# Optimization experiments

Measured on AMD Instinct MI355X. Metric: run time of the kernel, lower is better.

## Reference

```python
import jax, jax.numpy as jnp
import numpy as np

B, T, L, H, W = 8, 30000, 6, 128, 128
D_IN, C_DIM, HID, Z_DIM = 3, 32, 256, 128
MAX_DIM = 0.55


def setup_inputs() -> dict:
    key = jax.random.key(0)
    ks = jax.random.split(key, 12)
    p = jax.random.uniform(ks[0], (B, T, D_IN), dtype=jnp.float32)
    z = jax.random.normal(ks[1], (B, Z_DIM), dtype=jnp.float32)
    c = jax.random.normal(ks[2], (B, L, H, W, C_DIM), dtype=jnp.float32)
    # camera-like matrices: small rotation rows so projected coords stay in [-1, 1]
    C_mat = (jax.random.uniform(ks[3], (B, L, 4, 3), dtype=jnp.float32) - 0.5) * 0.3
    C_mat = C_mat.at[:, :, 3, :].set(1.0)  # row used as projection denominator
    fc_p_w = jax.random.normal(ks[4], (HID, D_IN), dtype=jnp.float32) * 0.1
    fc_p_b = jnp.zeros((HID,), jnp.float32)
    blk0_w0 = jax.random.normal(ks[5], (C_DIM, HID), dtype=jnp.float32) * 0.05
    blk0_b0 = jnp.zeros((C_DIM,), jnp.float32)
    blk0_w1 = jax.random.normal(ks[6], (C_DIM, C_DIM), dtype=jnp.float32) * 0.1
    blk0_b1 = jnp.zeros((C_DIM,), jnp.float32)
    blk0_ws = jax.random.normal(ks[7], (C_DIM, HID), dtype=jnp.float32) * 0.05
    blk_w0 = jax.random.normal(ks[8], (4, C_DIM, C_DIM), dtype=jnp.float32) * 0.1
    blk_b0 = jnp.zeros((4, C_DIM), jnp.float32)
    blk_w1 = jax.random.normal(ks[9], (4, C_DIM, C_DIM), dtype=jnp.float32) * 0.1
    blk_b1 = jnp.zeros((4, C_DIM), jnp.float32)
    fc_out_w = jax.random.normal(ks[10], (1, C_DIM), dtype=jnp.float32) * 0.1
    fc_out_b = jnp.zeros((1,), jnp.float32)
    return dict(p=p, z=z, c=c, C_mat=C_mat, fc_p_w=fc_p_w, fc_p_b=fc_p_b,
                blk0_w0=blk0_w0, blk0_b0=blk0_b0, blk0_w1=blk0_w1, blk0_b1=blk0_b1,
                blk0_ws=blk0_ws, blk_w0=blk_w0, blk_b0=blk_b0, blk_w1=blk_w1,
                blk_b1=blk_b1, fc_out_w=fc_out_w, fc_out_b=fc_out_b)


def _bilinear(p, c, C_mat):
    # p: [B,T,3], c: [B,L,H,W,D], C_mat: [B,L,4,3]
    Bb, Ll, Hh, Ww, Dd = c.shape
    interval = 2.0 / (Hh - 1)
    pp = p / MAX_DIM
    # proj[b,l,t,i] = sum_j C_mat[b,l,i,j] * pp[b,t,j]
    proj = jnp.einsum('blij,btj->blti', C_mat[:, :, :3, :], pp)
    denom = C_mat[:, :, 3, 0] + 0.05                      # [B,L]
    proj = proj / denom[:, :, None, None]
    xy = (proj[..., :2] + 1.0) / interval                 # [B,L,T,2]
    x, y = xy[..., 0], xy[..., 1]
    x0f, x1f = jnp.floor(x), jnp.ceil(x)
    y0f, y1f = jnp.floor(y), jnp.ceil(y)
    dx = (x1f - x)[..., None]                             # [B,L,T,1]
    dy = (y1f - y)[..., None]
    x0 = jnp.clip(x0f.astype(jnp.int32), 0, Hh - 1)
    x1 = jnp.clip(x1f.astype(jnp.int32), 0, Hh - 1)
    y0 = jnp.clip(y0f.astype(jnp.int32), 0, Ww - 1)
    y1 = jnp.clip(y1f.astype(jnp.int32), 0, Ww - 1)
    bi = jnp.arange(Bb)[:, None, None]
    li = jnp.arange(Ll)[None, :, None]
    f11 = c[bi, li, x0, y0]                               # [B,L,T,D]
    f12 = c[bi, li, x1, y0]
    f21 = c[bi, li, x0, y1]
    f22 = c[bi, li, x1, y1]
    interp = (f11 * dx * dy + f12 * (1 - dx) * dy
              + f21 * dx * (1 - dy) + f22 * (1 - dx) * (1 - dy))
    return interp.sum(axis=1)                             # sum over views -> [B,T,D]


def reference(p, z, c, C_mat, fc_p_w, fc_p_b, blk0_w0, blk0_b0, blk0_w1, blk0_b1,
              blk0_ws, blk_w0, blk_b0, blk_w1, blk_b1, fc_out_w, fc_out_b):
    feat = _bilinear(p, c, C_mat)                         # [B,T,32]
    net = p @ fc_p_w.T + fc_p_b                           # 1x1 conv == linear, [B,T,256]
    # block0 (256 -> 32, with linear shortcut)
    h = jax.nn.relu(net) @ blk0_w0.T + blk0_b0
    dx_ = jax.nn.relu(h) @ blk0_w1.T + blk0_b1
    net = net @ blk0_ws.T + dx_
    net = net + feat
    # blocks 1..4 (32 -> 32, identity shortcut)
    for i in range(4):
        h = jax.nn.relu(net) @ blk_w0[i].T + blk_b0[i]
        net = net + (jax.nn.relu(h) @ blk_w1[i].T + blk_b1[i])
        net = net + feat
    out = jax.nn.relu(net) @ fc_out_w.T + fc_out_b        # [B,T,1]
    return out[..., 0]                                    # [B,T]
```

## Files before the change

### kernel.cpp

```cpp
#include <hip/hip_runtime.h>

#define NB 8
#define NT 30000
#define NL 6
#define NC 32
#define NHID 256

typedef _Float16 f16;
typedef f16 half8 __attribute__((ext_vector_type(8)));
typedef f16 half4v __attribute__((ext_vector_type(4)));
typedef f16 half2v __attribute__((ext_vector_type(2)));
typedef float floatx4 __attribute__((ext_vector_type(4)));

__device__ __forceinline__ int permrow(int m) {
    return 8 * ((m & 15) >> 2) + 4 * (m >> 4) + (m & 3);
}

__device__ __forceinline__ half2v cvt2(float a, float b) {
    return __builtin_bit_cast(half2v, __builtin_amdgcn_cvt_pkrtz(a, b));
}

__device__ __forceinline__ half8 relupack2(floatx4 a, floatx4 b) {
    half2v p0 = cvt2(fmaxf(a[0], 0.f), fmaxf(a[1], 0.f));
    half2v p1 = cvt2(fmaxf(a[2], 0.f), fmaxf(a[3], 0.f));
    half2v p2 = cvt2(fmaxf(b[0], 0.f), fmaxf(b[1], 0.f));
    half2v p3 = cvt2(fmaxf(b[2], 0.f), fmaxf(b[3], 0.f));
    half4v q0 = __builtin_shufflevector(p0, p1, 0, 1, 2, 3);
    half4v q1 = __builtin_shufflevector(p2, p3, 0, 1, 2, 3);
    return __builtin_shufflevector(q0, q1, 0, 1, 2, 3, 4, 5, 6, 7);
}

__device__ __forceinline__ half8 zext4(half4v lo) {
    const half4v zh = {};
    return __builtin_shufflevector(lo, zh, 0, 1, 2, 3, 4, 5, 6, 7);
}

__global__ void fold_kernel(const float* __restrict__ ws, const float* __restrict__ fpw,
                            const float* __restrict__ fpb, floatx4* __restrict__ out) {
    __shared__ floatx4 s_part[8][32];
    int tid = threadIdx.x;
    int i = tid & 31, kc = tid >> 5;
    const float* wrow = ws + i * 256 + kc * 32;
    const float* pw = fpw + kc * 96;
    const float* pb = fpb + kc * 32;
    floatx4 acc = {};
    #pragma unroll 8
    for (int k = 0; k < 32; k++) {
        float w = wrow[k];
        acc[0] = fmaf(w, pw[k * 3 + 0], acc[0]);
        acc[1] = fmaf(w, pw[k * 3 + 1], acc[1]);
        acc[2] = fmaf(w, pw[k * 3 + 2], acc[2]);
        acc[3] = fmaf(w, pb[k], acc[3]);
    }
    s_part[kc][i] = acc;
    __syncthreads();
    if (kc == 0) {
        floatx4 s = s_part[0][i];
        #pragma unroll
        for (int j = 1; j < 8; j++) s += s_part[j][i];
        out[i] = s;
    }
}

__launch_bounds__(256, 2)
__global__ void decoder_kernel(
    const float* __restrict__ p, const float* __restrict__ c, const float* __restrict__ Cm,
    const float* __restrict__ fpw, const float* __restrict__ fpb,
    const float* __restrict__ b0w0, const float* __restrict__ b0b0,
    const float* __restrict__ b0w1, const float* __restrict__ b0b1,
    const float* __restrict__ bw0, const float* __restrict__ bb0,
    const float* __restrict__ bw1, const float* __restrict__ bb1,
    const float* __restrict__ fow, const float* __restrict__ fob,
    const floatx4* __restrict__ fold, float* __restrict__ out)
{
    __shared__ __align__(16) f16 s_w0A[32 * 256];
    __shared__ __align__(16) f16 s_wA[9 * 32 * 32];
    __shared__ __align__(16) f16 s_hB[256 * 4];
    __shared__ __align__(16) f16 s_foldA[32 * 4];
    __shared__ __align__(16) float s_b0b0[32], s_fow[32];
    __shared__ __align__(16) float s_bb0f[128], s_bb1f[128];
    __shared__ float s_cam[NL][8];
    __shared__ float s_fob;

    const int tid = threadIdx.x;
    const int b = blockIdx.y;

    {
        int m = tid >> 3, seg = tid & 7;
        const float* src = b0w0 + permrow(m) * 256 + seg * 32;
        f16* dst = s_w0A + m * 256;
        int sw = m & 7;
        #pragma unroll
        for (int ci = 0; ci < 4; ci++) {
            int cidx = seg * 4 + ci;
            floatx4 f0 = *(const floatx4*)(src + ci * 8);
            floatx4 f1 = *(const floatx4*)(src + ci * 8 + 4);
            half2v h0 = cvt2(f0[0], f0[1]), h1 = cvt2(f0[2], f0[3]);
            half2v h2 = cvt2(f1[0], f1[1]), h3 = cvt2(f1[2], f1[3]);
            half4v q0 = __builtin_shufflevector(h0, h1, 0, 1, 2, 3);
            half4v q1 = __builtin_shufflevector(h2, h3, 0, 1, 2, 3);
            half8 h = __builtin_shufflevector(q0, q1, 0, 1, 2, 3, 4, 5, 6, 7);
            *(half8*)(dst + ((cidx ^ sw) << 3)) = h;
        }
    }
    for (int r = tid; r < 288; r += 256) {
        int mi = r >> 5, m = r & 31;
        int pm = permrow(m);
        const float* src;
        if (mi == 0) src = b0w1 + pm * 32;
        else {
            int mat = mi - 1, bi = mat >> 1;
            src = ((mat & 1) ? bw1 : bw0) + (bi * 32 + pm) * 32;
        }
        f16* dst = s_wA + mi * 1024 + m * 32;
        int sw = (m >> 1) & 3;
        #pragma unroll
        for (int ci = 0; ci < 4; ci++) {
            floatx4 f0 = *(const floatx4*)(src + ci * 8);
            floatx4 f1 = *(const floatx4*)(src + ci * 8 + 4);
            half2v h0 = cvt2(f0[0], f0[1]), h1 = cvt2(f0[2], f0[3]);
            half2v h2 = cvt2(f1[0], f1[1]), h3 = cvt2(f1[2], f1[3]);
            half4v q0 = __builtin_shufflevector(h0, h1, 0, 1, 2, 3);
            half4v q1 = __builtin_shufflevector(h2, h3, 0, 1, 2, 3);
            half8 h = __builtin_shufflevector(q0, q1, 0, 1, 2, 3, 4, 5, 6, 7);
            *(half8*)(dst + ((ci ^ sw) << 3)) = h;
        }
    }
    {
        int cch = tid >> 5, m = tid & 31;
        int h = cch * 32 + permrow(m);
        half2v a = cvt2(fpw[h * 3 + 0], fpw[h * 3 + 1]);
        half2v bq = cvt2(fpw[h * 3 + 2], fpb[h]);
        *(half4v*)(s_hB + tid * 4) = __builtin_shufflevector(a, bq, 0, 1, 2, 3);
    }
    if (tid < 32) {
        int pm = permrow(tid);
        floatx4 f = fold[pm];
        half2v a = cvt2(f[0], f[1]);
        half2v bq = cvt2(f[2], f[3] + b0b1[pm]);
        *(half4v*)(s_foldA + tid * 4) = __builtin_shufflevector(a, bq, 0, 1, 2, 3);
        s_b0b0[tid] = b0b0[tid];
        s_fow[tid]  = fow[tid];
    }
    if (tid >= 64 && tid < 192) {
        int j = tid - 64;
        s_bb0f[j] = bb0[j];
        s_bb1f[j] = bb1[j];
    }
    if (tid == 0) s_fob = fob[0];
    if (tid >= 192 && tid < 192 + NL) {
        int l = tid - 192;
        const float* cm = Cm + ((size_t)b * NL + l) * 12;
        float denom = cm[9] + 0.05f;
        float s = 63.5f / (0.55f * denom);
        s_cam[l][0] = cm[0] * s; s_cam[l][1] = cm[1] * s; s_cam[l][2] = cm[2] * s;
        s_cam[l][3] = cm[3] * s; s_cam[l][4] = cm[4] * s; s_cam[l][5] = cm[5] * s;
    }
    __syncthreads();

    const int lane = tid & 63;
    const int wv = tid >> 6;
    const int q = lane >> 4;
    const int i16 = lane & 15;
    const int sw0 = i16 & 7;

    const f16* w0r0 = s_w0A + i16 * 256;
    const f16* w0r1 = s_w0A + (16 + i16) * 256;
    const int qsw = (q ^ ((i16 >> 1) & 3)) << 3;
    const int soff0 = i16 * 32 + qsw;
    const int soff1 = (16 + i16) * 32 + qsw;
    const f16* hB0 = s_hB + i16 * 4;
    const f16* hB1 = s_hB + (16 + i16) * 4;
    const float* cq = c + (((size_t)b * NL) << 19) + q * 8;

    const half8 fA0 = zext4(*(const half4v*)(s_foldA + i16 * 4));
    const half8 fA1 = zext4(*(const half4v*)(s_foldA + (16 + i16) * 4));
    const floatx4 fw0 = *(const floatx4*)&s_fow[q * 8];
    const floatx4 fw1 = *(const floatx4*)&s_fow[q * 8 + 4];
    const floatx4 b00a = *(const floatx4*)&s_b0b0[q * 8];
    const floatx4 b00b = *(const floatx4*)&s_b0b0[q * 8 + 4];

    #pragma unroll 1
    for (int g = 0; g < 2; g++) {
        const int t = blockIdx.x * 128 + (g * 4 + wv) * 16 + i16;
        const int tc = min(t, NT - 1);
        const float* pp = p + ((size_t)b * NT + tc) * 3;
        float px = pp[0], py = pp[1], pz = pp[2];

        floatx4 fe0 = {}, fe1 = {};
        #pragma unroll 1
        for (int l = 0; l < NL; l++) {
            float x = s_cam[l][0] * px + s_cam[l][1] * py + s_cam[l][2] * pz + 63.5f;
            float y = s_cam[l][3] * px + s_cam[l][4] * py + s_cam[l][5] * pz + 63.5f;
            float x0f = floorf(x), x1f = ceilf(x);
            float y0f = floorf(y), y1f = ceilf(y);
            float dxw = x1f - x, dyw = y1f - y;
            int x0 = min(max((int)x0f, 0), 127);
            int x1 = min(max((int)x1f, 0), 127);
            int y0 = min(max((int)y0f, 0), 127);
            int y1 = min(max((int)y1f, 0), 127);
            const float* base = cq + ((size_t)l << 19);
            const floatx4* f11 = (const floatx4*)(base + (size_t)((x0 << 7) + y0) * 32);
            const floatx4* f12 = (const floatx4*)(base + (size_t)((x1 << 7) + y0) * 32);
            const floatx4* f21 = (const floatx4*)(base + (size_t)((x0 << 7) + y1) * 32);
            const floatx4* f22 = (const floatx4*)(base + (size_t)((x1 << 7) + y1) * 32);
            float w11 = dxw * dyw;
            float w12 = (1.f - dxw) * dyw;
            float w21 = dxw * (1.f - dyw);
            float w22 = (1.f - dxw) * (1.f - dyw);
            floatx4 a0 = f11[0], a1 = f11[1];
            floatx4 b0v = f12[0], b1v = f12[1];
            floatx4 c0v = f21[0], c1v = f21[1];
            floatx4 d0v = f22[0], d1v = f22[1];
            fe0 += a0 * w11 + b0v * w12 + c0v * w21 + d0v * w22;
            fe1 += a1 * w11 + b1v * w12 + c1v * w21 + d1v * w22;
        }

        half8 bp;
        {
            half2v xy = cvt2(px, py), z1 = cvt2(pz, 1.0f);
            half4v lo = __builtin_shufflevector(xy, z1, 0, 1, 2, 3);
            half8 full = zext4(lo);
            const half8 zh8 = {};
            bp = (q == 0) ? full : zh8;
        }

        floatx4 acc0 = b00a, acc1 = b00b;
        #pragma unroll 2
        for (int cch = 0; cch < 8; cch++) {
            half8 ha = zext4(*(const half4v*)(hB0 + cch * 128));
            half8 hb = zext4(*(const half4v*)(hB1 + cch * 128));
            floatx4 hz = {};
            floatx4 h0 = __builtin_amdgcn_mfma_f32_16x16x32_f16(ha, bp, hz, 0, 0, 0);
            floatx4 h1 = __builtin_amdgcn_mfma_f32_16x16x32_f16(hb, bp, hz, 0, 0, 0);
            half8 bf = relupack2(h0, h1);
            half8 a0 = *(const half8*)(w0r0 + ((((cch << 2) | q) ^ sw0) << 3));
            half8 a1 = *(const half8*)(w0r1 + ((((cch << 2) | q) ^ sw0) << 3));
            acc0 = __builtin_amdgcn_mfma_f32_16x16x32_f16(a0, bf, acc0, 0, 0, 0);
            acc1 = __builtin_amdgcn_mfma_f32_16x16x32_f16(a1, bf, acc1, 0, 0, 0);
        }

        floatx4 st0 = __builtin_amdgcn_mfma_f32_16x16x32_f16(fA0, bp, fe0, 0, 0, 0);
        floatx4 st1 = __builtin_amdgcn_mfma_f32_16x16x32_f16(fA1, bp, fe1, 0, 0, 0);
        {
            half8 bf = relupack2(acc0, acc1);
            half8 a0 = *(const half8*)(s_wA + soff0);
            half8 a1 = *(const half8*)(s_wA + soff1);
            st0 = __builtin_amdgcn_mfma_f32_16x16x32_f16(a0, bf, st0, 0, 0, 0);
            st1 = __builtin_amdgcn_mfma_f32_16x16x32_f16(a1, bf, st1, 0, 0, 0);
        }

        #pragma unroll
        for (int bk = 0; bk < 4; bk++) {
            const f16* w_a = s_wA + (1 + 2 * bk) * 1024;
            const f16* w_b = s_wA + (2 + 2 * bk) * 1024;
            floatx4 h0 = *(const floatx4*)&s_bb0f[bk * 32 + q * 8];
            floatx4 h1 = *(const floatx4*)&s_bb0f[bk * 32 + q * 8 + 4];
            {
                half8 bf = relupack2(st0, st1);
                half8 a0 = *(const half8*)(w_a + soff0);
                half8 a1 = *(const half8*)(w_a + soff1);
                h0 = __builtin_amdgcn_mfma_f32_16x16x32_f16(a0, bf, h0, 0, 0, 0);
                h1 = __builtin_amdgcn_mfma_f32_16x16x32_f16(a1, bf, h1, 0, 0, 0);
            }
            floatx4 d0 = *(const floatx4*)&s_bb1f[bk * 32 + q * 8];
            floatx4 d1 = *(const floatx4*)&s_bb1f[bk * 32 + q * 8 + 4];
            {
                half8 bf = relupack2(h0, h1);
                half8 a0 = *(const half8*)(w_b + soff0);
                half8 a1 = *(const half8*)(w_b + soff1);
                d0 = __builtin_amdgcn_mfma_f32_16x16x32_f16(a0, bf, d0, 0, 0, 0);
                d1 = __builtin_amdgcn_mfma_f32_16x16x32_f16(a1, bf, d1, 0, 0, 0);
            }
            st0 += d0 + fe0;
            st1 += d1 + fe1;
        }

        float o = 0.f;
        #pragma unroll
        for (int r = 0; r < 4; r++)
            o += fmaxf(st0[r], 0.f) * fw0[r] + fmaxf(st1[r], 0.f) * fw1[r];
        o += __shfl_xor(o, 16);
        o += __shfl_xor(o, 32);
        if (q == 0 && t < NT) out[(size_t)b * NT + t] = o + s_fob;
    }
}

extern "C" void kernel_launch(void* const* d_in, const int* in_sizes, int n_in,
                              void* d_out, int out_size, void* d_ws, size_t ws_size,
                              hipStream_t stream) {
    const float* p    = (const float*)d_in[0];
    const float* c    = (const float*)d_in[2];
    const float* Cm   = (const float*)d_in[3];
    const float* fpw  = (const float*)d_in[4];
    const float* fpb  = (const float*)d_in[5];
    const float* b0w0 = (const float*)d_in[6];
    const float* b0b0 = (const float*)d_in[7];
    const float* b0w1 = (const float*)d_in[8];
    const float* b0b1 = (const float*)d_in[9];
    const float* b0ws = (const float*)d_in[10];
    const float* bw0  = (const float*)d_in[11];
    const float* bb0  = (const float*)d_in[12];
    const float* bw1  = (const float*)d_in[13];
    const float* bb1  = (const float*)d_in[14];
    const float* fow  = (const float*)d_in[15];
    const float* fob  = (const float*)d_in[16];
    floatx4* fold = (floatx4*)d_ws;

    fold_kernel<<<1, 256, 0, stream>>>(b0ws, fpw, fpb, fold);

    dim3 grid((NT + 127) / 128, NB);
    decoder_kernel<<<grid, 256, 0, stream>>>(p, c, Cm, fpw, fpb,
                                             b0w0, b0b0, b0w1, b0b1,
                                             bw0, bb0, bw1, bb1,
                                             fow, fob, fold, (float*)d_out);
}
```

Baseline: 267.4 us.

## Pre-convert feature grid to fp16 and stage weight image globally for decoder

```diff
diff --git a/kernel.cpp b/kernel.cpp
--- a/kernel.cpp
+++ b/kernel.cpp
@@ -12,12 +12,33 @@
 typedef f16 half2v __attribute__((ext_vector_type(2)));
 typedef float floatx4 __attribute__((ext_vector_type(4)));
 
+#define C_ELEMS (25165824ull)
+#define NCONV   12288
+
+#define OFF_W0A  0
+#define OFF_WA   8192
+#define OFF_HB   17408
+#define OFF_FOLD 18432
+#define OFF_F32  18560
+#define IMG_F16  19456
+
+__device__ __align__(16) f16 g_chalf[C_ELEMS];
+__device__ __align__(16) f16 g_img[IMG_F16];
+
 __device__ __forceinline__ int permrow(int m) {
     return 8 * ((m & 15) >> 2) + 4 * (m >> 4) + (m & 3);
 }
 
 __device__ __forceinline__ half2v cvt2(float a, float b) {
     return __builtin_bit_cast(half2v, __builtin_amdgcn_cvt_pkrtz(a, b));
+}
+
+__device__ __forceinline__ half8 pack8(floatx4 f0, floatx4 f1) {
+    half2v h0 = cvt2(f0[0], f0[1]), h1 = cvt2(f0[2], f0[3]);
+    half2v h2 = cvt2(f1[0], f1[1]), h3 = cvt2(f1[2], f1[3]);
+    half4v q0 = __builtin_shufflevector(h0, h1, 0, 1, 2, 3);
+    half4v q1 = __builtin_shufflevector(h2, h3, 0, 1, 2, 3);
+    return __builtin_shufflevector(q0, q1, 0, 1, 2, 3, 4, 5, 6, 7);
 }
 
 __device__ __forceinline__ half8 relupack2(floatx4 a, floatx4 b) {
@@ -35,72 +56,59 @@
     return __builtin_shufflevector(lo, zh, 0, 1, 2, 3, 4, 5, 6, 7);
 }
 
-__global__ void fold_kernel(const float* __restrict__ ws, const float* __restrict__ fpw,
-                            const float* __restrict__ fpb, floatx4* __restrict__ out) {
-    __shared__ floatx4 s_part[8][32];
-    int tid = threadIdx.x;
-    int i = tid & 31, kc = tid >> 5;
-    const float* wrow = ws + i * 256 + kc * 32;
-    const float* pw = fpw + kc * 96;
-    const float* pb = fpb + kc * 32;
-    floatx4 acc = {};
-    #pragma unroll 8
-    for (int k = 0; k < 32; k++) {
-        float w = wrow[k];
-        acc[0] = fmaf(w, pw[k * 3 + 0], acc[0]);
-        acc[1] = fmaf(w, pw[k * 3 + 1], acc[1]);
-        acc[2] = fmaf(w, pw[k * 3 + 2], acc[2]);
-        acc[3] = fmaf(w, pb[k], acc[3]);
-    }
-    s_part[kc][i] = acc;
-    __syncthreads();
-    if (kc == 0) {
-        floatx4 s = s_part[0][i];
-        #pragma unroll
-        for (int j = 1; j < 8; j++) s += s_part[j][i];
-        out[i] = s;
-    }
-}
-
-__launch_bounds__(256, 2)
-__global__ void decoder_kernel(
-    const float* __restrict__ p, const float* __restrict__ c, const float* __restrict__ Cm,
+__device__ __forceinline__ half8 splat8(float w) {
+    f16 h = (f16)w;
+    half8 v = {h, h, h, h, h, h, h, h};
+    return v;
+}
+
+__global__ __launch_bounds__(256) void convert_prep(
+    const float* __restrict__ c,
     const float* __restrict__ fpw, const float* __restrict__ fpb,
     const float* __restrict__ b0w0, const float* __restrict__ b0b0,
     const float* __restrict__ b0w1, const float* __restrict__ b0b1,
-    const float* __restrict__ bw0, const float* __restrict__ bb0,
-    const float* __restrict__ bw1, const float* __restrict__ bb1,
-    const float* __restrict__ fow, const float* __restrict__ fob,
-    const floatx4* __restrict__ fold, float* __restrict__ out)
+    const float* __restrict__ b0ws, const float* __restrict__ bw0,
+    const float* __restrict__ bb0, const float* __restrict__ bw1,
+    const float* __restrict__ bb1, const float* __restrict__ fow,
+    const float* __restrict__ fob)
 {
-    __shared__ __align__(16) f16 s_w0A[32 * 256];
-    __shared__ __align__(16) f16 s_wA[9 * 32 * 32];
-    __shared__ __align__(16) f16 s_hB[256 * 4];
-    __shared__ __align__(16) f16 s_foldA[32 * 4];
-    __shared__ __align__(16) float s_b0b0[32], s_fow[32];
-    __shared__ __align__(16) float s_bb0f[128], s_bb1f[128];
-    __shared__ float s_cam[NL][8];
-    __shared__ float s_fob;
-
+    __shared__ floatx4 sp[8][32];
     const int tid = threadIdx.x;
-    const int b = blockIdx.y;
-
+    if (blockIdx.x < NCONV) {
+        size_t i = ((size_t)blockIdx.x * 256 + tid) * 8;
+        floatx4 f0 = *(const floatx4*)(c + i);
+        floatx4 f1 = *(const floatx4*)(c + i + 4);
+        *(half8*)(g_chalf + i) = pack8(f0, f1);
+        return;
+    }
+    {
+        int i = tid & 31, kc = tid >> 5;
+        const float* wrow = b0ws + i * 256 + kc * 32;
+        const float* pw = fpw + kc * 96;
+        const float* pb = fpb + kc * 32;
+        floatx4 acc = {};
+        #pragma unroll 8
+        for (int k = 0; k < 32; k++) {
+            float w = wrow[k];
+            acc[0] = fmaf(w, pw[k * 3 + 0], acc[0]);
+            acc[1] = fmaf(w, pw[k * 3 + 1], acc[1]);
+            acc[2] = fmaf(w, pw[k * 3 + 2], acc[2]);
+            acc[3] = fmaf(w, pb[k], acc[3]);
+        }
+        sp[kc][i] = acc;
+    }
+    __syncthreads();
     {
         int m = tid >> 3, seg = tid & 7;
         const float* src = b0w0 + permrow(m) * 256 + seg * 32;
-        f16* dst = s_w0A + m * 256;
+        f16* dst = g_img + OFF_W0A + m * 256;
         int sw = m & 7;
         #pragma unroll
         for (int ci = 0; ci < 4; ci++) {
             int cidx = seg * 4 + ci;
             floatx4 f0 = *(const floatx4*)(src + ci * 8);
             floatx4 f1 = *(const floatx4*)(src + ci * 8 + 4);
-            half2v h0 = cvt2(f0[0], f0[1]), h1 = cvt2(f0[2], f0[3]);
-            half2v h2 = cvt2(f1[0], f1[1]), h3 = cvt2(f1[2], f1[3]);
-            half4v q0 = __builtin_shufflevector(h0, h1, 0, 1, 2, 3);
-            half4v q1 = __builtin_shufflevector(h2, h3, 0, 1, 2, 3);
-            half8 h = __builtin_shufflevector(q0, q1, 0, 1, 2, 3, 4, 5, 6, 7);
-            *(half8*)(dst + ((cidx ^ sw) << 3)) = h;
+            *(half8*)(dst + ((cidx ^ sw) << 3)) = pack8(f0, f1);
         }
     }
     for (int r = tid; r < 288; r += 256) {
@@ -112,18 +120,13 @@
             int mat = mi - 1, bi = mat >> 1;
             src = ((mat & 1) ? bw1 : bw0) + (bi * 32 + pm) * 32;
         }
-        f16* dst = s_wA + mi * 1024 + m * 32;
+        f16* dst = g_img + OFF_WA + mi * 1024 + m * 32;
         int sw = (m >> 1) & 3;
         #pragma unroll
         for (int ci = 0; ci < 4; ci++) {
             floatx4 f0 = *(const floatx4*)(src + ci * 8);
             floatx4 f1 = *(const floatx4*)(src + ci * 8 + 4);
-            half2v h0 = cvt2(f0[0], f0[1]), h1 = cvt2(f0[2], f0[3]);
-            half2v h2 = cvt2(f1[0], f1[1]), h3 = cvt2(f1[2], f1[3]);
-            half4v q0 = __builtin_shufflevector(h0, h1, 0, 1, 2, 3);
-            half4v q1 = __builtin_shufflevector(h2, h3, 0, 1, 2, 3);
-            half8 h = __builtin_shufflevector(q0, q1, 0, 1, 2, 3, 4, 5, 6, 7);
-            *(half8*)(dst + ((ci ^ sw) << 3)) = h;
+            *(half8*)(dst + ((ci ^ sw) << 3)) = pack8(f0, f1);
         }
     }
     {
@@ -131,23 +134,43 @@
         int h = cch * 32 + permrow(m);
         half2v a = cvt2(fpw[h * 3 + 0], fpw[h * 3 + 1]);
         half2v bq = cvt2(fpw[h * 3 + 2], fpb[h]);
-        *(half4v*)(s_hB + tid * 4) = __builtin_shufflevector(a, bq, 0, 1, 2, 3);
-    }
+        *(half4v*)(g_img + OFF_HB + tid * 4) = __builtin_shufflevector(a, bq, 0, 1, 2, 3);
+    }
+    float* fimg = (float*)(g_img + OFF_F32);
     if (tid < 32) {
         int pm = permrow(tid);
-        floatx4 f = fold[pm];
-        half2v a = cvt2(f[0], f[1]);
-        half2v bq = cvt2(f[2], f[3] + b0b1[pm]);
-        *(half4v*)(s_foldA + tid * 4) = __builtin_shufflevector(a, bq, 0, 1, 2, 3);
-        s_b0b0[tid] = b0b0[tid];
-        s_fow[tid]  = fow[tid];
+        floatx4 s = sp[0][pm];
+        #pragma unroll
+        for (int j = 1; j < 8; j++) s += sp[j][pm];
+        half2v a = cvt2(s[0], s[1]);
+        half2v bq = cvt2(s[2], s[3] + b0b1[pm]);
+        *(half4v*)(g_img + OFF_FOLD + tid * 4) = __builtin_shufflevector(a, bq, 0, 1, 2, 3);
+        fimg[tid] = b0b0[tid];
+        fimg[32 + tid] = fow[tid];
     }
     if (tid >= 64 && tid < 192) {
-        int j = tid - 64;
-        s_bb0f[j] = bb0[j];
-        s_bb1f[j] = bb1[j];
-    }
-    if (tid == 0) s_fob = fob[0];
+        fimg[tid] = bb0[tid - 64];
+        fimg[tid + 128] = bb1[tid - 64];
+    }
+    if (tid == 0) fimg[320] = fob[0];
+}
+
+__global__ __launch_bounds__(256, 4) void decoder_kernel(
+    const float* __restrict__ p, const float* __restrict__ Cm,
+    float* __restrict__ out)
+{
+    __shared__ __align__(16) f16 s_img[IMG_F16];
+    __shared__ float s_cam[NL][8];
+
+    const int tid = threadIdx.x;
+    const int b = blockIdx.x & 7;
+    const int tile = blockIdx.x >> 3;
+
+    {
+        const uint4* gsrc = (const uint4*)g_img;
+        uint4* ldst = (uint4*)s_img;
+        for (int i = tid; i < IMG_F16 / 8; i += 256) ldst[i] = gsrc[i];
+    }
     if (tid >= 192 && tid < 192 + NL) {
         int l = tid - 192;
         const float* cm = Cm + ((size_t)b * NL + l) * 12;
@@ -164,6 +187,11 @@
     const int i16 = lane & 15;
     const int sw0 = i16 & 7;
 
+    const f16* s_w0A = s_img + OFF_W0A;
+    const f16* s_wA  = s_img + OFF_WA;
+    const f16* s_hB  = s_img + OFF_HB;
+    const float* sf  = (const float*)(s_img + OFF_F32);
+
     const f16* w0r0 = s_w0A + i16 * 256;
     const f16* w0r1 = s_w0A + (16 + i16) * 256;
     const int qsw = (q ^ ((i16 >> 1) & 3)) << 3;
@@ -171,23 +199,24 @@
     const int soff1 = (16 + i16) * 32 + qsw;
     const f16* hB0 = s_hB + i16 * 4;
     const f16* hB1 = s_hB + (16 + i16) * 4;
-    const float* cq = c + (((size_t)b * NL) << 19) + q * 8;
-
-    const half8 fA0 = zext4(*(const half4v*)(s_foldA + i16 * 4));
-    const half8 fA1 = zext4(*(const half4v*)(s_foldA + (16 + i16) * 4));
-    const floatx4 fw0 = *(const floatx4*)&s_fow[q * 8];
-    const floatx4 fw1 = *(const floatx4*)&s_fow[q * 8 + 4];
-    const floatx4 b00a = *(const floatx4*)&s_b0b0[q * 8];
-    const floatx4 b00b = *(const floatx4*)&s_b0b0[q * 8 + 4];
+    const f16* cqh = g_chalf + (((size_t)b * NL) << 19) + q * 8;
+
+    const half8 fA0 = zext4(*(const half4v*)(s_img + OFF_FOLD + i16 * 4));
+    const half8 fA1 = zext4(*(const half4v*)(s_img + OFF_FOLD + (16 + i16) * 4));
+    const floatx4 fw0 = *(const floatx4*)&sf[32 + q * 8];
+    const floatx4 fw1 = *(const floatx4*)&sf[32 + q * 8 + 4];
+    const floatx4 b00a = *(const floatx4*)&sf[q * 8];
+    const floatx4 b00b = *(const floatx4*)&sf[q * 8 + 4];
+    const float fobv = sf[320];
 
     #pragma unroll 1
     for (int g = 0; g < 2; g++) {
-        const int t = blockIdx.x * 128 + (g * 4 + wv) * 16 + i16;
+        const int t = tile * 128 + (g * 4 + wv) * 16 + i16;
         const int tc = min(t, NT - 1);
         const float* pp = p + ((size_t)b * NT + tc) * 3;
         float px = pp[0], py = pp[1], pz = pp[2];
 
-        floatx4 fe0 = {}, fe1 = {};
+        half8 feh = {};
         #pragma unroll 1
         for (int l = 0; l < NL; l++) {
             float x = s_cam[l][0] * px + s_cam[l][1] * py + s_cam[l][2] * pz + 63.5f;
@@ -199,22 +228,20 @@
             int x1 = min(max((int)x1f, 0), 127);
             int y0 = min(max((int)y0f, 0), 127);
             int y1 = min(max((int)y1f, 0), 127);
-            const float* base = cq + ((size_t)l << 19);
-            const floatx4* f11 = (const floatx4*)(base + (size_t)((x0 << 7) + y0) * 32);
-            const floatx4* f12 = (const floatx4*)(base + (size_t)((x1 << 7) + y0) * 32);
-            const floatx4* f21 = (const floatx4*)(base + (size_t)((x0 << 7) + y1) * 32);
-            const floatx4* f22 = (const floatx4*)(base + (size_t)((x1 << 7) + y1) * 32);
+            const f16* base = cqh + ((size_t)l << 19);
+            half8 t11 = *(const half8*)(base + (size_t)((x0 << 7) + y0) * 32);
+            half8 t12 = *(const half8*)(base + (size_t)((x1 << 7) + y0) * 32);
+            half8 t21 = *(const half8*)(base + (size_t)((x0 << 7) + y1) * 32);
+            half8 t22 = *(const half8*)(base + (size_t)((x1 << 7) + y1) * 32);
             float w11 = dxw * dyw;
             float w12 = (1.f - dxw) * dyw;
             float w21 = dxw * (1.f - dyw);
             float w22 = (1.f - dxw) * (1.f - dyw);
-            floatx4 a0 = f11[0], a1 = f11[1];
-            floatx4 b0v = f12[0], b1v = f12[1];
-            floatx4 c0v = f21[0], c1v = f21[1];
-            floatx4 d0v = f22[0], d1v = f22[1];
-            fe0 += a0 * w11 + b0v * w12 + c0v * w21 + d0v * w22;
-            fe1 += a1 * w11 + b1v * w12 + c1v * w21 + d1v * w22;
-        }
+            feh += t11 * splat8(w11) + t12 * splat8(w12)
+                 + t21 * splat8(w21) + t22 * splat8(w22);
+        }
+        floatx4 fe0 = floatx4{(float)feh[0], (float)feh[1], (float)feh[2], (float)feh[3]};
+        floatx4 fe1 = floatx4{(float)feh[4], (float)feh[5], (float)feh[6], (float)feh[7]};
 
         half8 bp;
         {
@@ -254,8 +281,8 @@
         for (int bk = 0; bk < 4; bk++) {
             const f16* w_a = s_wA + (1 + 2 * bk) * 1024;
             const f16* w_b = s_wA + (2 + 2 * bk) * 1024;
-            floatx4 h0 = *(const floatx4*)&s_bb0f[bk * 32 + q * 8];
-            floatx4 h1 = *(const floatx4*)&s_bb0f[bk * 32 + q * 8 + 4];
+            floatx4 h0 = *(const floatx4*)&sf[64 + bk * 32 + q * 8];
+            floatx4 h1 = *(const floatx4*)&sf[64 + bk * 32 + q * 8 + 4];
             {
                 half8 bf = relupack2(st0, st1);
                 half8 a0 = *(const half8*)(w_a + soff0);
@@ -263,8 +290,8 @@
                 h0 = __builtin_amdgcn_mfma_f32_16x16x32_f16(a0, bf, h0, 0, 0, 0);
                 h1 = __builtin_amdgcn_mfma_f32_16x16x32_f16(a1, bf, h1, 0, 0, 0);
             }
-            floatx4 d0 = *(const floatx4*)&s_bb1f[bk * 32 + q * 8];
-            floatx4 d1 = *(const floatx4*)&s_bb1f[bk * 32 + q * 8 + 4];
+            floatx4 d0 = *(const floatx4*)&sf[192 + bk * 32 + q * 8];
+            floatx4 d1 = *(const floatx4*)&sf[192 + bk * 32 + q * 8 + 4];
             {
                 half8 bf = relupack2(h0, h1);
                 half8 a0 = *(const half8*)(w_b + soff0);
@@ -282,7 +309,7 @@
             o += fmaxf(st0[r], 0.f) * fw0[r] + fmaxf(st1[r], 0.f) * fw1[r];
         o += __shfl_xor(o, 16);
         o += __shfl_xor(o, 32);
-        if (q == 0 && t < NT) out[(size_t)b * NT + t] = o + s_fob;
+        if (q == 0 && t < NT) out[(size_t)b * NT + t] = o + fobv;
     }
 }
 
@@ -305,13 +332,10 @@
     const float* bb1  = (const float*)d_in[14];
     const float* fow  = (const float*)d_in[15];
     const float* fob  = (const float*)d_in[16];
-    floatx4* fold = (floatx4*)d_ws;
-
-    fold_kernel<<<1, 256, 0, stream>>>(b0ws, fpw, fpb, fold);
-
-    dim3 grid((NT + 127) / 128, NB);
-    decoder_kernel<<<grid, 256, 0, stream>>>(p, c, Cm, fpw, fpb,
-                                             b0w0, b0b0, b0w1, b0b1,
-                                             bw0, bb0, bw1, bb1,
-                                             fow, fob, fold, (float*)d_out);
-}
+
+    convert_prep<<<NCONV + 1, 256, 0, stream>>>(c, fpw, fpb, b0w0, b0b0, b0w1, b0b1,
+                                                b0ws, bw0, bb0, bw1, bb1, fow, fob);
+
+    dim3 grid(((NT + 127) / 128) * NB);
+    decoder_kernel<<<grid, 256, 0, stream>>>(p, Cm, (float*)d_out);
+}
```

New measurement: 298.3 us. +11.6%, slower.
